# Optimization experiments

Measured on AMD Instinct MI355X. Metric: run time of the kernel, lower is better.

The kernel has to match this reference:

```python
import jax, jax.numpy as jnp
import numpy as np

T, H, I, E, TOPK = 1024, 1024, 2816, 16, 4


def setup_inputs() -> dict:
    key = jax.random.key(0)
    ks = jax.random.split(key, 5)
    s_h = 1.0 / np.sqrt(H)
    s_i = 1.0 / np.sqrt(I)
    return {
        "x": jax.random.normal(ks[0], (T, H), jnp.float32),
        "Wg": jax.random.normal(ks[1], (E, H), jnp.float32) * s_h,
        "gate_w": jax.random.normal(ks[2], (E, H, I), jnp.float32) * s_h,
        "up_w": jax.random.normal(ks[3], (E, H, I), jnp.float32) * s_h,
        "down_w": jax.random.normal(ks[4], (E, I, H), jnp.float32) * s_i,
        "top_k": TOPK,
    }


def reference(x, Wg, gate_w, up_w, down_w, top_k):
    # Router: softmax over expert logits, top-k, renormalize
    logits = x @ Wg.T                                   # [T, E]
    probs = jax.nn.softmax(logits, axis=-1)
    topk_w, topk_ids = jax.lax.top_k(probs, top_k)      # [T, K]
    topk_w = topk_w / jnp.sum(topk_w, axis=-1, keepdims=True)

    # Dense combine weights [T, E]: zero for unselected experts -> exact same
    # math as the per-token dispatch loop in the original module.
    n_tok = x.shape[0]
    combine = jnp.zeros((n_tok, Wg.shape[0]), x.dtype)
    combine = combine.at[jnp.arange(n_tok)[:, None], topk_ids].add(topk_w)

    # SwiGLU per expert, batched over the expert axis
    g = jax.nn.silu(jnp.einsum('th,ehi->eti', x, gate_w))  # [E, T, I]
    u = jnp.einsum('th,ehi->eti', x, up_w)                 # [E, T, I]
    y = jnp.einsum('eti,eih->eth', g * u, down_w)          # [E, T, H]

    # Weighted combine across experts
    return jnp.einsum('eth,te->th', y, combine)            # [T, H]
```

## Files before the change

### kernel.cpp

```cpp
#include <hip/hip_runtime.h>

static constexpr int cT = 1024;
static constexpr int cH = 1024;
static constexpr int cI = 2816;
static constexpr int cE = 16;
static constexpr int cK = 4;

typedef __attribute__((ext_vector_type(8))) short bf16x8;
typedef __attribute__((ext_vector_type(4))) float f32x4;
typedef __attribute__((ext_vector_type(2))) unsigned uint2v;
typedef __attribute__((ext_vector_type(4))) unsigned uint4v;

__device__ __forceinline__ unsigned f2bf(float f) {
  unsigned u = __float_as_uint(f);
  return (u + 0x7FFFu + ((u >> 16) & 1u)) >> 16;
}
__device__ __forceinline__ unsigned pack2(float lo, float hi) {
  return f2bf(lo) | (f2bf(hi) << 16);
}

__global__ __launch_bounds__(256) void xcast_kernel(
    const float* __restrict__ x, unsigned short* __restrict__ xb) {
  const int i = blockIdx.x * 256 + threadIdx.x;
  const float4* xv = (const float4*)x;
  const float4 a = xv[i * 2], b = xv[i * 2 + 1];
  uint4v o;
  o.x = pack2(a.x, a.y); o.y = pack2(a.z, a.w);
  o.z = pack2(b.x, b.y); o.w = pack2(b.z, b.w);
  ((uint4v*)xb)[i] = o;
}

__global__ __launch_bounds__(64) void router_kernel(
    const float* __restrict__ x, const float* __restrict__ Wg,
    int* __restrict__ topk_id, float* __restrict__ topk_w,
    int* __restrict__ counts) {
  const int t = blockIdx.x;
  const int l = threadIdx.x;

  float xa[16];
#pragma unroll
  for (int i = 0; i < 16; ++i) xa[i] = x[(size_t)t * cH + l + 64 * i];

  float lg[16];
#pragma unroll
  for (int e = 0; e < 16; ++e) {
    float s = 0.f;
#pragma unroll
    for (int i = 0; i < 16; ++i) s += xa[i] * Wg[(size_t)e * cH + l + 64 * i];
#pragma unroll
    for (int d = 1; d < 64; d <<= 1) s += __shfl_xor(s, d);
    lg[e] = s;
  }

  if (l == 0) {
    int ids[4]; float vals[4];
    unsigned taken = 0;
#pragma unroll
    for (int j = 0; j < 4; ++j) {
      float m = -1e30f; int mi = 0;
#pragma unroll
      for (int e = 0; e < 16; ++e) {
        bool better = !((taken >> e) & 1u) && lg[e] > m;
        if (better) { m = lg[e]; mi = e; }
      }
      taken |= 1u << mi; ids[j] = mi; vals[j] = m;
    }
    const float mx = vals[0];
    float s = 0.f;
#pragma unroll
    for (int j = 0; j < 4; ++j) { vals[j] = __expf(vals[j] - mx); s += vals[j]; }
    const float inv = 1.f / s;
#pragma unroll
    for (int j = 0; j < 4; ++j) {
      topk_id[t * 4 + j] = ids[j];
      topk_w[t * 4 + j] = vals[j] * inv;
      atomicAdd(&counts[ids[j]], 1);
    }
  }
}

__global__ void scan_kernel(const int* __restrict__ counts,
                            int* __restrict__ offsets) {
  if (threadIdx.x == 0 && blockIdx.x == 0) {
    int acc = 0;
    for (int e = 0; e < cE; ++e) { offsets[e] = acc; acc += counts[e]; }
    offsets[cE] = acc;
  }
}

__global__ __launch_bounds__(256) void scatter_kernel(
    const int* __restrict__ topk_id, const int* __restrict__ offsets,
    int* __restrict__ cursor, int* __restrict__ pair_token,
    int* __restrict__ pair_pos) {
  const int i = blockIdx.x * 256 + threadIdx.x;
  const int t = i >> 2;
  const int e = topk_id[i];
  const int pos = offsets[e] + atomicAdd(&cursor[e], 1);
  pair_token[pos] = t;
  pair_pos[i] = pos;
}


__global__ __launch_bounds__(256, 3) void gateup_kernel(
    const unsigned short* __restrict__ xb, const float* __restrict__ gw,
    const float* __restrict__ uw, const int* __restrict__ offsets,
    const int* __restrict__ pair_token, unsigned short* __restrict__ actT) {
  const int e = blockIdx.y;
  const int off = offsets[e];
  const int n_e = offsets[e + 1] - off;
  const int strip = blockIdx.x / 3;
  const int c0 = (blockIdx.x % 3) * 128;
  if (c0 >= n_e) return;
  const int nb = strip * 64;
  const int tid = threadIdx.x, l = tid & 63, w = tid >> 6;
  const int q = l & 15, h16 = l >> 4;
  const int hrd = 2 * ((q >> 2) & 3);

  __shared__ unsigned sB[2][2][2304];
  __shared__ int tokl[128];

  const int mat = tid >> 7, tt = tid & 127, rg = tt >> 4, cg = tt & 15;
  const int hwr = 2 * (cg & 3);
  const float* wsrc = (mat ? uw : gw) + (size_t)e * cH * cI + nb + cg * 4;

#define GU_LDSET(S, KT)                                                       \
  _Pragma("unroll")                                                           \
  for (int j = 0; j < 8; ++j)                                                 \
    S[j] = *(const float4*)(wsrc + (size_t)((KT) * 64 + rg * 8 + j) * cI);

#define GU_PACK(BUF, S)                                                       \
  _Pragma("unroll")                                                           \
  for (int i = 0; i < 4; ++i) {                                               \
    uint4v P;                                                                 \
    P.x = pack2(S[0][i], S[1][i]); P.y = pack2(S[2][i], S[3][i]);             \
    P.z = pack2(S[4][i], S[5][i]); P.w = pack2(S[6][i], S[7][i]);             \
    *(uint4v*)&sB[BUF][mat][(4 * cg + i) * 36 + 4 * ((rg + hwr) & 7)] = P;    \
  }

#define GU_TILE(KT, CUR, SC, SN)                                              \
  {                                                                           \
    if ((KT) + 2 < 16) { GU_LDSET(SC, (KT) + 2) }                             \
    _Pragma("unroll")                                                         \
    for (int ks = 0; ks < 2; ++ks) {                                          \
      const bf16x8 a0 = *(const bf16x8*)(ap0 + (KT) * 64 + ks * 32);          \
      const bf16x8 a1 = *(const bf16x8*)(ap1 + (KT) * 64 + ks * 32);          \
      _Pragma("unroll")                                                       \
      for (int ni = 0; ni < 4; ++ni) {                                        \
        const int ba = (q + 16 * ni) * 36 + 4 * ((h16 + 4 * ks + hrd) & 7);   \
        const bf16x8 bg = *(const bf16x8*)&sB[CUR][0][ba];                    \
        const bf16x8 bu = *(const bf16x8*)&sB[CUR][1][ba];                    \
        ag0[ni] = __builtin_amdgcn_mfma_f32_16x16x32_bf16(a0, bg, ag0[ni], 0, 0, 0); \
        ag1[ni] = __builtin_amdgcn_mfma_f32_16x16x32_bf16(a1, bg, ag1[ni], 0, 0, 0); \
        au0[ni] = __builtin_amdgcn_mfma_f32_16x16x32_bf16(a0, bu, au0[ni], 0, 0, 0); \
        au1[ni] = __builtin_amdgcn_mfma_f32_16x16x32_bf16(a1, bu, au1[ni], 0, 0, 0); \
      }                                                                       \
    }                                                                         \
    if ((KT) + 1 < 16) { GU_PACK(1 - (CUR), SN) __syncthreads(); }            \
  }

  for (int m0 = c0; m0 < n_e; m0 += 384) {
    if (tid < 128) tokl[tid] = pair_token[off + min(m0 + tid, n_e - 1)];
    __syncthreads();
    const int rows = min(128, n_e - m0);

    const unsigned short* ap0 =
        xb + (size_t)tokl[min(w * 32 + q, rows - 1)] * cH + h16 * 8;
    const unsigned short* ap1 =
        xb + (size_t)tokl[min(w * 32 + 16 + q, rows - 1)] * cH + h16 * 8;

    f32x4 ag0[4], ag1[4], au0[4], au1[4];
#pragma unroll
    for (int ni = 0; ni < 4; ++ni) {
      ag0[ni] = (f32x4){0.f, 0.f, 0.f, 0.f}; ag1[ni] = (f32x4){0.f, 0.f, 0.f, 0.f};
      au0[ni] = (f32x4){0.f, 0.f, 0.f, 0.f}; au1[ni] = (f32x4){0.f, 0.f, 0.f, 0.f};
    }

    float4 s0[8], s1[8];
    GU_LDSET(s0, 0)
    GU_LDSET(s1, 1)
    GU_PACK(0, s0)
    __syncthreads();

    for (int kt = 0; kt < 16; kt += 2) {
      GU_TILE(kt, 0, s0, s1)
      GU_TILE(kt + 1, 1, s1, s0)
    }

#define GU_EPI(MI, AGV, AUV)                                                  \
  _Pragma("unroll")                                                           \
  for (int j = 0; j < 4; ++j) {                                               \
    const int er = m0 + w * 32 + (MI) * 16 + h16 * 4 + j;                     \
    if (er < n_e) {                                                           \
      const int p = off + er;                                                 \
      const size_t pb = (size_t)(p >> 4) * 45056 + (p & 15) * 8 +             \
                        (size_t)(nb >> 3) * 128 + (q & 7);                    \
      _Pragma("unroll")                                                       \
      for (int ni = 0; ni < 4; ++ni) {                                        \
        const float g = AGV[ni][j], u = AUV[ni][j];                           \
        const float v = (g / (1.f + __expf(-g))) * u;                         \
        actT[pb + (size_t)(ni * 2 + (q >> 3)) * 128] = (unsigned short)f2bf(v); \
      }                                                                       \
    }                                                                         \
  }
    GU_EPI(0, ag0, au0)
    GU_EPI(1, ag1, au1)
  }
#undef GU_LDSET
#undef GU_PACK
#undef GU_TILE
#undef GU_EPI
}

__global__ __launch_bounds__(256, 4) void down_kernel(
    const unsigned short* __restrict__ actT, const float* __restrict__ dw,
    const int* __restrict__ offsets, float* __restrict__ yp) {
  const int e = blockIdx.y;
  const int off = offsets[e];
  const int n_e = offsets[e + 1] - off;
  const int strip = blockIdx.x / 3;
  const int c0 = (blockIdx.x % 3) * 128;
  if (c0 >= n_e) return;
  const int nb = strip * 64;
  const int tid = threadIdx.x, l = tid & 63, w = tid >> 6;
  const int q = l & 15, h16 = l >> 4;
  const int hrd = 2 * ((q >> 2) & 3);
  constexpr int NT = cI / 64;

  __shared__ unsigned sB[2][2304];

  const int rg = tid >> 5, cg = (tid >> 1) & 15, half = tid & 1;
  const int hwr = 2 * (cg & 3);
  const float* dsrc = dw + (size_t)e * cI * cH + nb + cg * 4 + half * 2;

#define DN_LDSET(S, KT)                                                       \
  _Pragma("unroll")                                                           \
  for (int j = 0; j < 8; ++j)                                                 \
    S[j] = *(const float2*)(dsrc + (size_t)((KT) * 64 + rg * 8 + j) * cH);

#define DN_PACK(BUF, S)                                                       \
  _Pragma("unroll")                                                           \
  for (int i = 0; i < 2; ++i) {                                               \
    uint4v P;                                                                 \
    const float* Sf = (const float*)S;                                        \
    P.x = pack2(Sf[0 * 2 + i], Sf[1 * 2 + i]);                                \
    P.y = pack2(Sf[2 * 2 + i], Sf[3 * 2 + i]);                                \
    P.z = pack2(Sf[4 * 2 + i], Sf[5 * 2 + i]);                                \
    P.w = pack2(Sf[6 * 2 + i], Sf[7 * 2 + i]);                                \
    *(uint4v*)&sB[BUF][(4 * cg + 2 * half + i) * 36 + 4 * ((rg + hwr) & 7)] = P; \
  }

#define DN_TILE(KT, CUR, SC, SN)                                              \
  {                                                                           \
    if ((KT) + 2 < NT) { DN_LDSET(SC, (KT) + 2) }                             \
    _Pragma("unroll")                                                         \
    for (int ks = 0; ks < 2; ++ks) {                                          \
      const bf16x8 a0 = *(const bf16x8*)(actT + b0 + (size_t)((KT) * 8 + h16 + 4 * ks) * 128); \
      const bf16x8 a1 = *(const bf16x8*)(actT + b1 + (size_t)((KT) * 8 + h16 + 4 * ks) * 128); \
      _Pragma("unroll")                                                       \
      for (int ni = 0; ni < 4; ++ni) {                                        \
        const int ba = (q + 16 * ni) * 36 + 4 * ((h16 + 4 * ks + hrd) & 7);   \
        const bf16x8 b = *(const bf16x8*)&sB[CUR][ba];                        \
        ac0[ni] = __builtin_amdgcn_mfma_f32_16x16x32_bf16(a0, b, ac0[ni], 0, 0, 0); \
        ac1[ni] = __builtin_amdgcn_mfma_f32_16x16x32_bf16(a1, b, ac1[ni], 0, 0, 0); \
      }                                                                       \
    }                                                                         \
    if ((KT) + 1 < NT) { DN_PACK(1 - (CUR), SN) __syncthreads(); }            \
  }

  for (int m0 = c0; m0 < n_e; m0 += 384) {
    const int p0g = off + min(m0 + w * 32 + q, n_e - 1);
    const int p1g = off + min(m0 + w * 32 + 16 + q, n_e - 1);
    const size_t b0 = (size_t)(p0g >> 4) * 45056 + (p0g & 15) * 8;
    const size_t b1 = (size_t)(p1g >> 4) * 45056 + (p1g & 15) * 8;

    f32x4 ac0[4], ac1[4];
#pragma unroll
    for (int ni = 0; ni < 4; ++ni) {
      ac0[ni] = (f32x4){0.f, 0.f, 0.f, 0.f};
      ac1[ni] = (f32x4){0.f, 0.f, 0.f, 0.f};
    }

    float2 s0[8], s1[8];
    DN_LDSET(s0, 0)
    DN_LDSET(s1, 1)
    DN_PACK(0, s0)
    __syncthreads();

    for (int kt = 0; kt < NT; kt += 2) {
      DN_TILE(kt, 0, s0, s1)
      DN_TILE(kt + 1, 1, s1, s0)
    }

#define DN_EPI(MI, ACV)                                                       \
  _Pragma("unroll")                                                           \
  for (int j = 0; j < 4; ++j) {                                               \
    const int er = m0 + w * 32 + (MI) * 16 + h16 * 4 + j;                     \
    if (er < n_e) {                                                           \
      _Pragma("unroll")                                                       \
      for (int ni = 0; ni < 4; ++ni)                                          \
        yp[(size_t)(off + er) * cH + nb + ni * 16 + q] = ACV[ni][j];          \
    }                                                                         \
  }
    DN_EPI(0, ac0)
    DN_EPI(1, ac1)

    if (m0 + 384 < n_e) __syncthreads();
  }
#undef DN_LDSET
#undef DN_PACK
#undef DN_TILE
#undef DN_EPI
}

__global__ __launch_bounds__(256) void combine_kernel(
    const float* __restrict__ yp, const int* __restrict__ pair_pos,
    const float* __restrict__ topk_w, float* __restrict__ out) {
  const int t = blockIdx.x;
  const int cb = threadIdx.x * 4;
  float4 s = make_float4(0.f, 0.f, 0.f, 0.f);
#pragma unroll
  for (int j = 0; j < 4; ++j) {
    const int pos = pair_pos[t * 4 + j];
    const float wj = topk_w[t * 4 + j];
    const float4 v = *(const float4*)(yp + (size_t)pos * cH + cb);
    s.x += wj * v.x; s.y += wj * v.y; s.z += wj * v.z; s.w += wj * v.w;
  }
  *(float4*)(out + (size_t)t * cH + cb) = s;
}

extern "C" void kernel_launch(void* const* d_in, const int* in_sizes, int n_in,
                              void* d_out, int out_size, void* d_ws,
                              size_t ws_size, hipStream_t stream) {
  (void)in_sizes; (void)n_in; (void)out_size; (void)ws_size;
  const float* x = (const float*)d_in[0];
  const float* Wg = (const float*)d_in[1];
  const float* gw = (const float*)d_in[2];
  const float* uw = (const float*)d_in[3];
  const float* dw = (const float*)d_in[4];
  float* out = (float*)d_out;

  char* ws = (char*)d_ws;
  int* counts     = (int*)(ws + 0);
  int* cursor     = (int*)(ws + 64);
  int* offsets    = (int*)(ws + 128);
  int* topk_id    = (int*)(ws + 256);
  float* topk_w   = (float*)(ws + 256 + 16384);
  int* pair_token = (int*)(ws + 256 + 32768);
  int* pair_pos   = (int*)(ws + 256 + 49152);
  unsigned short* actT = (unsigned short*)(ws + 65792);
  unsigned short* xb   = (unsigned short*)(ws + 65792 + (size_t)4096 * 2816 * 2);
  float* yp = (float*)(ws + 65792 + (size_t)4096 * 2816 * 2 + (size_t)cT * cH * 2);

  hipMemsetAsync(ws, 0, 128, stream);

  xcast_kernel<<<cT * cH / (256 * 8), 256, 0, stream>>>(x, xb);
  router_kernel<<<cT, 64, 0, stream>>>(x, Wg, topk_id, topk_w, counts);
  scan_kernel<<<1, 1, 0, stream>>>(counts, offsets);
  scatter_kernel<<<cT * cK / 256, 256, 0, stream>>>(topk_id, offsets, cursor,
                                                    pair_token, pair_pos);
  gateup_kernel<<<dim3(44 * 3, cE), 256, 0, stream>>>(xb, gw, uw, offsets,
                                                      pair_token, actT);
  down_kernel<<<dim3(16 * 3, cE), 256, 0, stream>>>(actT, dw, offsets, yp);
  combine_kernel<<<cT, 256, 0, stream>>>(yp, pair_pos, topk_w, out);
}
```

Measured before the change: 491.1 us.

## Switch activation to row-major, stage A tiles in LDS, widen down-proj tile

The intermediate activation moves from a custom blocked-transposed layout to plain row-major [pairs, I]. The down kernel now stages activation tiles into swizzled LDS alongside the weights and doubles its output column tile from 64 to 128, halving the grid and dropping occupancy hint to 2. The gate/up kernel reshapes its weight loading so every thread loads both gate and up with a padded stride of 34, and its software pipeline is restructured. The aim is fewer redundant dw reads and more coalesced activation loads, at the cost of more registers and LDS per block.

```diff
diff --git a/kernel.cpp b/kernel.cpp
--- a/kernel.cpp
+++ b/kernel.cpp
@@ -17,6 +17,13 @@
 }
 __device__ __forceinline__ unsigned pack2(float lo, float hi) {
   return f2bf(lo) | (f2bf(hi) << 16);
+}
+
+__device__ __forceinline__ bf16x8 ld_bfrag(const unsigned* p) {
+  union { uint2v d[2]; bf16x8 v; } r;
+  r.d[0] = *(const uint2v*)p;
+  r.d[1] = *(const uint2v*)(p + 2);
+  return r.v;
 }
 
 __global__ __launch_bounds__(256) void xcast_kernel(
@@ -100,11 +107,10 @@
   pair_pos[i] = pos;
 }
 
-
 __global__ __launch_bounds__(256, 3) void gateup_kernel(
     const unsigned short* __restrict__ xb, const float* __restrict__ gw,
     const float* __restrict__ uw, const int* __restrict__ offsets,
-    const int* __restrict__ pair_token, unsigned short* __restrict__ actT) {
+    const int* __restrict__ pair_token, unsigned short* __restrict__ act) {
   const int e = blockIdx.y;
   const int off = offsets[e];
   const int n_e = offsets[e + 1] - off;
@@ -114,48 +120,48 @@
   const int nb = strip * 64;
   const int tid = threadIdx.x, l = tid & 63, w = tid >> 6;
   const int q = l & 15, h16 = l >> 4;
-  const int hrd = 2 * ((q >> 2) & 3);
-
-  __shared__ unsigned sB[2][2][2304];
+
+  __shared__ unsigned sB[2][2][2176];
   __shared__ int tokl[128];
 
-  const int mat = tid >> 7, tt = tid & 127, rg = tt >> 4, cg = tt & 15;
-  const int hwr = 2 * (cg & 3);
-  const float* wsrc = (mat ? uw : gw) + (size_t)e * cH * cI + nb + cg * 4;
-
-#define GU_LDSET(S, KT)                                                       \
-  _Pragma("unroll")                                                           \
-  for (int j = 0; j < 8; ++j)                                                 \
-    S[j] = *(const float4*)(wsrc + (size_t)((KT) * 64 + rg * 8 + j) * cI);
-
-#define GU_PACK(BUF, S)                                                       \
+  const int sa = tid >> 4, sc = tid & 15;
+  const float* gb = gw + (size_t)e * cH * cI + nb + sc * 4;
+  const float* ub = uw + (size_t)e * cH * cI + nb + sc * 4;
+
+  float4 g0[4], u0[4], g1[4], u1[4];
+
+#define GU_LD(G, U, KT)                                                       \
+  _Pragma("unroll")                                                           \
+  for (int j = 0; j < 4; ++j) {                                               \
+    G[j] = *(const float4*)(gb + (size_t)((KT) * 64 + sa * 4 + j) * cI);      \
+    U[j] = *(const float4*)(ub + (size_t)((KT) * 64 + sa * 4 + j) * cI);      \
+  }
+
+#define GU_PACK(BUF, G, U)                                                    \
   _Pragma("unroll")                                                           \
   for (int i = 0; i < 4; ++i) {                                               \
-    uint4v P;                                                                 \
-    P.x = pack2(S[0][i], S[1][i]); P.y = pack2(S[2][i], S[3][i]);             \
-    P.z = pack2(S[4][i], S[5][i]); P.w = pack2(S[6][i], S[7][i]);             \
-    *(uint4v*)&sB[BUF][mat][(4 * cg + i) * 36 + 4 * ((rg + hwr) & 7)] = P;    \
-  }
-
-#define GU_TILE(KT, CUR, SC, SN)                                              \
-  {                                                                           \
-    if ((KT) + 2 < 16) { GU_LDSET(SC, (KT) + 2) }                             \
+    uint2v pg, pu;                                                            \
+    pg.x = pack2(G[0][i], G[1][i]); pg.y = pack2(G[2][i], G[3][i]);           \
+    pu.x = pack2(U[0][i], U[1][i]); pu.y = pack2(U[2][i], U[3][i]);           \
+    *(uint2v*)&sB[BUF][0][(sc * 4 + i) * 34 + sa * 2] = pg;                   \
+    *(uint2v*)&sB[BUF][1][(sc * 4 + i) * 34 + sa * 2] = pu;                   \
+  }
+
+#define GU_MFMA(CUR, KT)                                                      \
+  _Pragma("unroll")                                                           \
+  for (int ks = 0; ks < 2; ++ks) {                                            \
+    const bf16x8 a0 = *(const bf16x8*)(ap0 + (KT) * 64 + ks * 32);            \
+    const bf16x8 a1 = *(const bf16x8*)(ap1 + (KT) * 64 + ks * 32);            \
     _Pragma("unroll")                                                         \
-    for (int ks = 0; ks < 2; ++ks) {                                          \
-      const bf16x8 a0 = *(const bf16x8*)(ap0 + (KT) * 64 + ks * 32);          \
-      const bf16x8 a1 = *(const bf16x8*)(ap1 + (KT) * 64 + ks * 32);          \
-      _Pragma("unroll")                                                       \
-      for (int ni = 0; ni < 4; ++ni) {                                        \
-        const int ba = (q + 16 * ni) * 36 + 4 * ((h16 + 4 * ks + hrd) & 7);   \
-        const bf16x8 bg = *(const bf16x8*)&sB[CUR][0][ba];                    \
-        const bf16x8 bu = *(const bf16x8*)&sB[CUR][1][ba];                    \
-        ag0[ni] = __builtin_amdgcn_mfma_f32_16x16x32_bf16(a0, bg, ag0[ni], 0, 0, 0); \
-        ag1[ni] = __builtin_amdgcn_mfma_f32_16x16x32_bf16(a1, bg, ag1[ni], 0, 0, 0); \
-        au0[ni] = __builtin_amdgcn_mfma_f32_16x16x32_bf16(a0, bu, au0[ni], 0, 0, 0); \
-        au1[ni] = __builtin_amdgcn_mfma_f32_16x16x32_bf16(a1, bu, au1[ni], 0, 0, 0); \
-      }                                                                       \
+    for (int ni = 0; ni < 4; ++ni) {                                          \
+      const int ba = (q + 16 * ni) * 34 + h16 * 4 + 16 * ks;                  \
+      const bf16x8 bg = ld_bfrag(&sB[CUR][0][ba]);                            \
+      const bf16x8 bu = ld_bfrag(&sB[CUR][1][ba]);                            \
+      ag0[ni] = __builtin_amdgcn_mfma_f32_16x16x32_bf16(a0, bg, ag0[ni], 0, 0, 0); \
+      ag1[ni] = __builtin_amdgcn_mfma_f32_16x16x32_bf16(a1, bg, ag1[ni], 0, 0, 0); \
+      au0[ni] = __builtin_amdgcn_mfma_f32_16x16x32_bf16(a0, bu, au0[ni], 0, 0, 0); \
+      au1[ni] = __builtin_amdgcn_mfma_f32_16x16x32_bf16(a1, bu, au1[ni], 0, 0, 0); \
     }                                                                         \
-    if ((KT) + 1 < 16) { GU_PACK(1 - (CUR), SN) __syncthreads(); }            \
   }
 
   for (int m0 = c0; m0 < n_e; m0 += 384) {
@@ -175,15 +181,22 @@
       au0[ni] = (f32x4){0.f, 0.f, 0.f, 0.f}; au1[ni] = (f32x4){0.f, 0.f, 0.f, 0.f};
     }
 
-    float4 s0[8], s1[8];
-    GU_LDSET(s0, 0)
-    GU_LDSET(s1, 1)
-    GU_PACK(0, s0)
+    GU_LD(g0, u0, 0)
+    GU_LD(g1, u1, 1)
+    GU_PACK(0, g0, u0)
     __syncthreads();
 
     for (int kt = 0; kt < 16; kt += 2) {
-      GU_TILE(kt, 0, s0, s1)
-      GU_TILE(kt + 1, 1, s1, s0)
+      if (kt + 2 < 16) { GU_LD(g0, u0, kt + 2) }
+      GU_MFMA(0, kt)
+      GU_PACK(1, g1, u1)
+      __syncthreads();
+      if (kt + 3 < 16) { GU_LD(g1, u1, kt + 3) }
+      GU_MFMA(1, kt + 1)
+      if (kt + 2 < 16) {
+        GU_PACK(0, g0, u0)
+        __syncthreads();
+      }
     }
 
 #define GU_EPI(MI, AGV, AUV)                                                  \
@@ -191,28 +204,26 @@
   for (int j = 0; j < 4; ++j) {                                               \
     const int er = m0 + w * 32 + (MI) * 16 + h16 * 4 + j;                     \
     if (er < n_e) {                                                           \
-      const int p = off + er;                                                 \
-      const size_t pb = (size_t)(p >> 4) * 45056 + (p & 15) * 8 +             \
-                        (size_t)(nb >> 3) * 128 + (q & 7);                    \
       _Pragma("unroll")                                                       \
       for (int ni = 0; ni < 4; ++ni) {                                        \
         const float g = AGV[ni][j], u = AUV[ni][j];                           \
         const float v = (g / (1.f + __expf(-g))) * u;                         \
-        actT[pb + (size_t)(ni * 2 + (q >> 3)) * 128] = (unsigned short)f2bf(v); \
+        act[(size_t)(off + er) * cI + nb + ni * 16 + q] =                     \
+            (unsigned short)f2bf(v);                                          \
       }                                                                       \
     }                                                                         \
   }
     GU_EPI(0, ag0, au0)
     GU_EPI(1, ag1, au1)
   }
-#undef GU_LDSET
+#undef GU_LD
 #undef GU_PACK
-#undef GU_TILE
+#undef GU_MFMA
 #undef GU_EPI
 }
 
-__global__ __launch_bounds__(256, 4) void down_kernel(
-    const unsigned short* __restrict__ actT, const float* __restrict__ dw,
+__global__ __launch_bounds__(256, 2) void down_kernel(
+    const unsigned short* __restrict__ act, const float* __restrict__ dw,
     const int* __restrict__ offsets, float* __restrict__ yp) {
   const int e = blockIdx.y;
   const int off = offsets[e];
@@ -220,75 +231,95 @@
   const int strip = blockIdx.x / 3;
   const int c0 = (blockIdx.x % 3) * 128;
   if (c0 >= n_e) return;
-  const int nb = strip * 64;
+  const int nb = strip * 128;
   const int tid = threadIdx.x, l = tid & 63, w = tid >> 6;
   const int q = l & 15, h16 = l >> 4;
-  const int hrd = 2 * ((q >> 2) & 3);
   constexpr int NT = cI / 64;
 
-  __shared__ unsigned sB[2][2304];
-
-  const int rg = tid >> 5, cg = (tid >> 1) & 15, half = tid & 1;
-  const int hwr = 2 * (cg & 3);
-  const float* dsrc = dw + (size_t)e * cI * cH + nb + cg * 4 + half * 2;
-
-#define DN_LDSET(S, KT)                                                       \
+  __shared__ unsigned sB[2][4352];
+  __shared__ unsigned short sA[2][8192];
+
+  const int rg = tid >> 5, cg = tid & 31;
+  const float* db = dw + (size_t)e * cI * cH + nb + cg * 4;
+
+  const int sr = tid >> 3, ss = tid & 7;
+  const int wslot = (ss ^ (sr & 7)) << 3;
+
+  const int rxor = q & 7;
+  const int r0base = (w * 32 + q) * 64;
+  const int r1base = r0base + 16 * 64;
+
+  float4 d0[8], d1[8];
+  uint4v a0s[4], a1s[4];
+
+#define DN_LDW(D, KT)                                                         \
   _Pragma("unroll")                                                           \
   for (int j = 0; j < 8; ++j)                                                 \
-    S[j] = *(const float2*)(dsrc + (size_t)((KT) * 64 + rg * 8 + j) * cH);
-
-#define DN_PACK(BUF, S)                                                       \
-  _Pragma("unroll")                                                           \
-  for (int i = 0; i < 2; ++i) {                                               \
-    uint4v P;                                                                 \
-    const float* Sf = (const float*)S;                                        \
-    P.x = pack2(Sf[0 * 2 + i], Sf[1 * 2 + i]);                                \
-    P.y = pack2(Sf[2 * 2 + i], Sf[3 * 2 + i]);                                \
-    P.z = pack2(Sf[4 * 2 + i], Sf[5 * 2 + i]);                                \
-    P.w = pack2(Sf[6 * 2 + i], Sf[7 * 2 + i]);                                \
-    *(uint4v*)&sB[BUF][(4 * cg + 2 * half + i) * 36 + 4 * ((rg + hwr) & 7)] = P; \
-  }
-
-#define DN_TILE(KT, CUR, SC, SN)                                              \
-  {                                                                           \
-    if ((KT) + 2 < NT) { DN_LDSET(SC, (KT) + 2) }                             \
+    D[j] = *(const float4*)(db + (size_t)((KT) * 64 + rg * 8 + j) * cH);
+
+#define DN_LDA(A, KT)                                                         \
+  _Pragma("unroll")                                                           \
+  for (int rd = 0; rd < 4; ++rd)                                              \
+    A[rd] = *(const uint4v*)(aptr[rd] + (KT) * 64);
+
+#define DN_PACK(BUF, D, A)                                                    \
+  _Pragma("unroll")                                                           \
+  for (int i = 0; i < 4; ++i) {                                               \
+    uint2v plo, phi;                                                          \
+    plo.x = pack2(D[0][i], D[1][i]); plo.y = pack2(D[2][i], D[3][i]);         \
+    phi.x = pack2(D[4][i], D[5][i]); phi.y = pack2(D[6][i], D[7][i]);         \
+    *(uint2v*)&sB[BUF][(cg * 4 + i) * 34 + rg * 4] = plo;                     \
+    *(uint2v*)&sB[BUF][(cg * 4 + i) * 34 + rg * 4 + 2] = phi;                 \
+  }                                                                           \
+  _Pragma("unroll")                                                           \
+  for (int rd = 0; rd < 4; ++rd)                                              \
+    *(uint4v*)&sA[BUF][(sr + rd * 32) * 64 + wslot] = A[rd];
+
+#define DN_MFMA(CUR)                                                          \
+  _Pragma("unroll")                                                           \
+  for (int ks = 0; ks < 2; ++ks) {                                            \
+    const int sl = ((h16 + 4 * ks) ^ rxor) << 3;                              \
+    const bf16x8 a0 = *(const bf16x8*)&sA[CUR][r0base + sl];                  \
+    const bf16x8 a1 = *(const bf16x8*)&sA[CUR][r1base + sl];                  \
     _Pragma("unroll")                                                         \
-    for (int ks = 0; ks < 2; ++ks) {                                          \
-      const bf16x8 a0 = *(const bf16x8*)(actT + b0 + (size_t)((KT) * 8 + h16 + 4 * ks) * 128); \
-      const bf16x8 a1 = *(const bf16x8*)(actT + b1 + (size_t)((KT) * 8 + h16 + 4 * ks) * 128); \
-      _Pragma("unroll")                                                       \
-      for (int ni = 0; ni < 4; ++ni) {                                        \
-        const int ba = (q + 16 * ni) * 36 + 4 * ((h16 + 4 * ks + hrd) & 7);   \
-        const bf16x8 b = *(const bf16x8*)&sB[CUR][ba];                        \
-        ac0[ni] = __builtin_amdgcn_mfma_f32_16x16x32_bf16(a0, b, ac0[ni], 0, 0, 0); \
-        ac1[ni] = __builtin_amdgcn_mfma_f32_16x16x32_bf16(a1, b, ac1[ni], 0, 0, 0); \
-      }                                                                       \
+    for (int ni = 0; ni < 8; ++ni) {                                          \
+      const bf16x8 b = ld_bfrag(&sB[CUR][(q + 16 * ni) * 34 + h16 * 4 + 16 * ks]); \
+      ac0[ni] = __builtin_amdgcn_mfma_f32_16x16x32_bf16(a0, b, ac0[ni], 0, 0, 0);  \
+      ac1[ni] = __builtin_amdgcn_mfma_f32_16x16x32_bf16(a1, b, ac1[ni], 0, 0, 0);  \
     }                                                                         \
-    if ((KT) + 1 < NT) { DN_PACK(1 - (CUR), SN) __syncthreads(); }            \
   }
 
   for (int m0 = c0; m0 < n_e; m0 += 384) {
-    const int p0g = off + min(m0 + w * 32 + q, n_e - 1);
-    const int p1g = off + min(m0 + w * 32 + 16 + q, n_e - 1);
-    const size_t b0 = (size_t)(p0g >> 4) * 45056 + (p0g & 15) * 8;
-    const size_t b1 = (size_t)(p1g >> 4) * 45056 + (p1g & 15) * 8;
-
-    f32x4 ac0[4], ac1[4];
-#pragma unroll
-    for (int ni = 0; ni < 4; ++ni) {
+    const unsigned short* aptr[4];
+#pragma unroll
+    for (int rd = 0; rd < 4; ++rd) {
+      const int p = off + min(m0 + sr + rd * 32, n_e - 1);
+      aptr[rd] = act + (size_t)p * cI + ss * 8;
+    }
+
+    f32x4 ac0[8], ac1[8];
+#pragma unroll
+    for (int ni = 0; ni < 8; ++ni) {
       ac0[ni] = (f32x4){0.f, 0.f, 0.f, 0.f};
       ac1[ni] = (f32x4){0.f, 0.f, 0.f, 0.f};
     }
 
-    float2 s0[8], s1[8];
-    DN_LDSET(s0, 0)
-    DN_LDSET(s1, 1)
-    DN_PACK(0, s0)
+    DN_LDW(d0, 0) DN_LDA(a0s, 0)
+    DN_LDW(d1, 1) DN_LDA(a1s, 1)
+    DN_PACK(0, d0, a0s)
     __syncthreads();
 
     for (int kt = 0; kt < NT; kt += 2) {
-      DN_TILE(kt, 0, s0, s1)
-      DN_TILE(kt + 1, 1, s1, s0)
+      if (kt + 2 < NT) { DN_LDW(d0, kt + 2) DN_LDA(a0s, kt + 2) }
+      DN_MFMA(0)
+      DN_PACK(1, d1, a1s)
+      __syncthreads();
+      if (kt + 3 < NT) { DN_LDW(d1, kt + 3) DN_LDA(a1s, kt + 3) }
+      DN_MFMA(1)
+      if (kt + 2 < NT) {
+        DN_PACK(0, d0, a0s)
+        __syncthreads();
+      }
     }
 
 #define DN_EPI(MI, ACV)                                                       \
@@ -297,7 +328,7 @@
     const int er = m0 + w * 32 + (MI) * 16 + h16 * 4 + j;                     \
     if (er < n_e) {                                                           \
       _Pragma("unroll")                                                       \
-      for (int ni = 0; ni < 4; ++ni)                                          \
+      for (int ni = 0; ni < 8; ++ni)                                          \
         yp[(size_t)(off + er) * cH + nb + ni * 16 + q] = ACV[ni][j];          \
     }                                                                         \
   }
@@ -306,9 +337,10 @@
 
     if (m0 + 384 < n_e) __syncthreads();
   }
-#undef DN_LDSET
+#undef DN_LDW
+#undef DN_LDA
 #undef DN_PACK
-#undef DN_TILE
+#undef DN_MFMA
 #undef DN_EPI
 }
 
@@ -347,8 +379,8 @@
   float* topk_w   = (float*)(ws + 256 + 16384);
   int* pair_token = (int*)(ws + 256 + 32768);
   int* pair_pos   = (int*)(ws + 256 + 49152);
-  unsigned short* actT = (unsigned short*)(ws + 65792);
-  unsigned short* xb   = (unsigned short*)(ws + 65792 + (size_t)4096 * 2816 * 2);
+  unsigned short* act = (unsigned short*)(ws + 65792);
+  unsigned short* xb  = (unsigned short*)(ws + 65792 + (size_t)4096 * 2816 * 2);
   float* yp = (float*)(ws + 65792 + (size_t)4096 * 2816 * 2 + (size_t)cT * cH * 2);
 
   hipMemsetAsync(ws, 0, 128, stream);
@@ -359,7 +391,7 @@
   scatter_kernel<<<cT * cK / 256, 256, 0, stream>>>(topk_id, offsets, cursor,
                                                     pair_token, pair_pos);
   gateup_kernel<<<dim3(44 * 3, cE), 256, 0, stream>>>(xb, gw, uw, offsets,
-                                                      pair_token, actT);
-  down_kernel<<<dim3(16 * 3, cE), 256, 0, stream>>>(actT, dw, offsets, yp);
+                                                      pair_token, act);
+  down_kernel<<<dim3(8 * 3, cE), 256, 0, stream>>>(act, dw, offsets, yp);
   combine_kernel<<<cT, 256, 0, stream>>>(yp, pair_pos, topk_w, out);
 }
```

New measurement: 532.3 us. 1.08x slower.
